# Performance work log

Measured on AMD Instinct MI355X. Metric: run time of the kernel, lower is better.

The kernel has to match this reference:

```python
import jax, jax.numpy as jnp
import numpy as np

B, L, E, H, W = 2, 4096, 512, 8, 128
D = E // H

def _clin(x, Wr, Wi, br, bi):
    # ComplexLinear on real input: out = x@(Wr + i*Wi)^T + (br + i*bi)
    return x @ Wr.T + br, x @ Wi.T + bi

def setup_inputs() -> dict:
    key = jax.random.key(0)
    ks = jax.random.split(key, 20)
    s = 0.02
    d = {
        'query': jax.random.normal(ks[0], (B, L, E), jnp.float32),
        'key':   jax.random.normal(ks[1], (B, L, E), jnp.float32),
        'value': jax.random.normal(ks[2], (B, L, E), jnp.float32),
    }
    names = ['q', 'k', 'v', 'o']
    i = 3
    for n in names:
        d[n + 'Wr'] = jax.random.normal(ks[i], (E, E), jnp.float32) * s; i += 1
        d[n + 'Wi'] = jax.random.normal(ks[i], (E, E), jnp.float32) * s; i += 1
        d[n + 'br'] = jnp.zeros((E,), jnp.float32)
        d[n + 'bi'] = jnp.zeros((E,), jnp.float32)
    return d

def reference(query, key, value,
              qWr, qWi, qbr, qbi,
              kWr, kWi, kbr, kbi,
              vWr, vWi, vbr, vbi,
              oWr, oWi, obr, obi):
    # complex projections (real input -> complex output, kept as (re, im) float pairs)
    qr, qi = _clin(query, qWr, qWi, qbr, qbi)
    kr, ki = _clin(key,   kWr, kWi, kbr, kbi)
    vr, _vi = _clin(value, vWr, vWi, vbr, vbi)  # imag part of V is discarded by the real cast

    def heads(x):
        return x.reshape(B, L, H, D).transpose(0, 2, 1, 3)  # [B,H,L,D]
    qr, qi, kr, ki, vr = map(heads, (qr, qi, kr, ki, vr))

    # Re(q @ k^H) = qr@kr^T + qi@ki^T  (only the real part is ever used)
    scale = 1.0 / np.sqrt(D)
    scores = (jnp.einsum('bhld,bhmd->bhlm', qr, kr)
              + jnp.einsum('bhld,bhmd->bhlm', qi, ki)) * scale

    # Faithful to source: only lower_mask is applied (window_mask is built but never added).
    idx = jnp.arange(L)
    lower_mask = jnp.where(idx[:, None] - idx[None, :] >= W + 1,
                           -jnp.inf, 0.0).astype(scores.dtype)
    probs = jax.nn.softmax(scores + lower_mask, axis=-1)

    # out = probs @ v; cast to query.dtype keeps only Re = probs @ vr
    o = jnp.einsum('bhlm,bhmd->bhld', probs, vr)
    o = o.transpose(0, 2, 1, 3).reshape(B, L, E)

    out_r = o @ oWr.T + obr
    out_i = o @ oWi.T + obi
    return out_r, out_i
```

## Files before the change

kernel.cpp:

```cpp
#include <hip/hip_runtime.h>


typedef unsigned short u16;
typedef unsigned int u32;
typedef __attribute__((ext_vector_type(8))) short bf16x8;
typedef __attribute__((ext_vector_type(4))) float f32x4;
typedef __attribute__((ext_vector_type(16))) float f32x16;
typedef __attribute__((ext_vector_type(4))) u32 u32x4;

#define L_ 4096
#define E_ 512
#define M_ 8192

__device__ __forceinline__ u16 f2bf(float f) {
  union { float f; u32 u; } v; v.f = f;
  return (u16)((v.u + 0x7FFFu + ((v.u >> 16) & 1u)) >> 16);
}

__device__ __forceinline__ void gll16(const void* g, void* l) {
  __builtin_amdgcn_global_load_lds(
      (const __attribute__((address_space(1))) u32*)g,
      (__attribute__((address_space(3))) u32*)l, 16, 0, 0);
}

__global__ void cvt_x_kernel(const float* __restrict__ q, const float* __restrict__ k,
                             const float* __restrict__ v,
                             u16* __restrict__ xq, u16* __restrict__ xk, u16* __restrict__ xv) {
  const int total = 3 * (M_ * E_ / 4);
  int stride = gridDim.x * blockDim.x;
  for (int u = blockIdx.x * blockDim.x + threadIdx.x; u < total; u += stride) {
    int mat = u >> 20, e = u & ((1 << 20) - 1);
    const float4 f = ((const float4*)(mat == 0 ? q : mat == 1 ? k : v))[e];
    ushort4 o = make_ushort4(f2bf(f.x), f2bf(f.y), f2bf(f.z), f2bf(f.w));
    *(ushort4*)((mat == 0 ? xq : mat == 1 ? xk : xv) + (size_t)e * 4) = o;
  }
}

struct CPtrs { const float* w[7]; const float* b[7]; };

__global__ void cvt_wb_kernel(CPtrs p, u16* __restrict__ wcat, float* __restrict__ bcat) {
  const int total = 7 * (E_ * E_ / 4);
  int stride = gridDim.x * blockDim.x;
  int t0 = blockIdx.x * blockDim.x + threadIdx.x;
  for (int u = t0; u < total; u += stride) {
    int wi = u >> 16, e = u & 65535;
    const float4 f = ((const float4*)p.w[wi])[e];
    ushort4 o = make_ushort4(f2bf(f.x), f2bf(f.y), f2bf(f.z), f2bf(f.w));
    *(ushort4*)(wcat + (size_t)wi * 262144 + (size_t)e * 4) = o;
  }
  for (int j = t0; j < 3584; j += stride) bcat[j] = p.b[j >> 9][j & 511];
}

__device__ __forceinline__ void gemm128_main(const u16* __restrict__ A, const u16* __restrict__ Bw,
                                             int m0, int n0w, char* sm, f32x4 acc[4][4]) {
  int tid = threadIdx.x;
  int lane = tid & 63, w = tid >> 6;
  int wm = w >> 1, wn = w & 1;
#pragma unroll
  for (int a = 0; a < 4; a++)
#pragma unroll
    for (int b = 0; b < 4; b++)
#pragma unroll
      for (int j = 0; j < 4; j++) acc[a][b][j] = 0.f;

  auto stage = [&](int buf, int ks) {
    char* dst = sm + buf * 16384;
#pragma unroll
    for (int n = 0; n < 2; n++) {
      int u = n * 256 + tid;
      int row = u >> 2, c = u & 3;
      int so = (c ^ (row & 3)) * 16;
      int ldso = (n * 256 + w * 64) * 16;
      gll16((const char*)(A + (size_t)(m0 + row) * 512 + ks * 32) + so, dst + ldso);
      gll16((const char*)(Bw + (size_t)(n0w + row) * 512 + ks * 32) + so, dst + 8192 + ldso);
    }
  };

  stage(0, 0);
  __syncthreads();
  int cur = 0;
  for (int ks = 0; ks < 16; ks++) {
    if (ks < 15) stage(cur ^ 1, ks + 1);
    const char* as = sm + cur * 16384;
    const char* bs = as + 8192;
    bf16x8 af[4], bfr[4];
#pragma unroll
    for (int i = 0; i < 4; i++) {
      int ra = wm * 64 + i * 16 + (lane & 15);
      af[i] = *(const bf16x8*)(as + ra * 64 + (((lane >> 4) * 16) ^ ((ra & 3) << 4)));
      int rb = wn * 64 + i * 16 + (lane & 15);
      bfr[i] = *(const bf16x8*)(bs + rb * 64 + (((lane >> 4) * 16) ^ ((rb & 3) << 4)));
    }
    __builtin_amdgcn_s_setprio(1);
#pragma unroll
    for (int mt = 0; mt < 4; mt++)
#pragma unroll
      for (int nt = 0; nt < 4; nt++)
        acc[mt][nt] = __builtin_amdgcn_mfma_f32_16x16x32_bf16(af[mt], bfr[nt], acc[mt][nt], 0, 0, 0);
    __builtin_amdgcn_s_setprio(0);
    __syncthreads();
    cur ^= 1;
  }
}

__global__ __launch_bounds__(256) void proj_kernel(
    const u16* __restrict__ xq, const u16* __restrict__ xk, const u16* __restrict__ xv,
    const u16* __restrict__ wcat, const float* __restrict__ bcat,
    u16* __restrict__ qrb, u16* __restrict__ qib,
    u16* __restrict__ krb, u16* __restrict__ kib, u16* __restrict__ vtb) {
  __shared__ alignas(16) char sm[32768];
  int bx = blockIdx.x, by = blockIdx.y;
  const u16* A = bx < 8 ? xq : (bx < 16 ? xk : xv);
  int m0 = by * 128, n0w = bx * 128;
  f32x4 acc[4][4];
  gemm128_main(A, wcat, m0, n0w, sm, acc);

  int lane = threadIdx.x & 63, w = threadIdx.x >> 6;
  int wm = w >> 1, wn = w & 1;
  int lL = lane & 15, lH = lane >> 4;
#pragma unroll
  for (int mt = 0; mt < 4; mt++) {
#pragma unroll
    for (int nt = 0; nt < 4; nt++) {
      int n = n0w + wn * 64 + nt * 16 + lL;
      float bias = bcat[n];
      int e = n & 511;
#pragma unroll
      for (int j = 0; j < 4; j++) {
        int m = m0 + wm * 64 + mt * 16 + lH * 4 + j;
        float val = acc[mt][nt][j] + bias;
        int bb = m >> 12, ll = m & 4095;
        if (bx < 16) {
          if (bx < 8) val *= 0.18033688011112042f;
          u16* dst = (bx < 8) ? ((n & 512) ? qib : qrb) : ((n & 512) ? kib : krb);
          dst[((size_t)((bb * 8 + (e >> 6)) * 4096 + ll) << 6) + (e & 63)] = f2bf(val);
        } else {
          vtb[((size_t)((bb * 8 + (e >> 6)) * 64 + (e & 63)) << 12) + ll] = f2bf(val);
        }
      }
    }
  }
}

__global__ __launch_bounds__(256) void oproj_kernel(
    const u16* __restrict__ obf, const u16* __restrict__ wcat, const float* __restrict__ bcat,
    float* __restrict__ out) {
  __shared__ alignas(16) char sm[32768];
  int bx = blockIdx.x, by = blockIdx.y;
  int m0 = by * 128, n0w = 2560 + bx * 128;
  f32x4 acc[4][4];
  gemm128_main(obf, wcat, m0, n0w, sm, acc);

  int lane = threadIdx.x & 63, w = threadIdx.x >> 6;
  int wm = w >> 1, wn = w & 1;
  int lL = lane & 15, lH = lane >> 4;
#pragma unroll
  for (int mt = 0; mt < 4; mt++) {
#pragma unroll
    for (int nt = 0; nt < 4; nt++) {
      int n = n0w + wn * 64 + nt * 16 + lL;
      float bias = bcat[n];
      int nn = n - 2560;
      float* dst = out + ((nn & 512) ? 4194304 : 0) + (nn & 511);
#pragma unroll
      for (int j = 0; j < 4; j++) {
        int m = m0 + wm * 64 + mt * 16 + lH * 4 + j;
        dst[(size_t)m * 512] = acc[mt][nt][j] + bias;
      }
    }
  }
}

__global__ __launch_bounds__(256, 2) void attn_kernel(
    const u16* __restrict__ qrb, const u16* __restrict__ qib,
    const u16* __restrict__ krb, const u16* __restrict__ kib,
    const u16* __restrict__ vtb, u16* __restrict__ obf) {
  __shared__ alignas(16) char sm[3 * 24576];
  int bid = blockIdx.x;
  int bh = bid & 15;
  int q2 = bid >> 4;
  int qt = (q2 < 16) ? q2 : (47 - q2);
  int bb = bh >> 3, hh = bh & 7;
  int i0 = qt << 7;
  int tid = threadIdx.x;
  int lane = tid & 63, w = tid >> 6;
  int lo = lane & 31, hi = lane >> 5;
  int i0w = i0 + w * 32;
  int irow = i0w + lo;

  bf16x8 fqr[4], fqi[4];
  {
    const u16* qp = qrb + ((size_t)(bh * 4096 + irow) << 6) + hi * 8;
    const u16* qip = qib + ((size_t)(bh * 4096 + irow) << 6) + hi * 8;
#pragma unroll
    for (int c = 0; c < 4; c++) {
      fqr[c] = *(const bf16x8*)(qp + c * 16);
      fqi[c] = *(const bf16x8*)(qip + c * 16);
    }
  }

  f32x16 oa0, oa1;
#pragma unroll
  for (int r = 0; r < 16; r++) { oa0[r] = 0.f; oa1[r] = 0.f; }
  float m_run = -1e30f, l_run = 0.f;

  int jstart = (i0 >= 128) ? (i0 - 128) : 0;
  int ntiles = (4096 - jstart) >> 6;

  auto stage = [&](char* dst, int j0) {
#pragma unroll
    for (int n = 0; n < 2; n++) {
      int u = n * 256 + tid;
      int row = u >> 3, c = u & 7;
      int so = (c ^ (row & 7)) * 16;
      int ldso = (n * 256 + w * 64) * 16;
      size_t krow = ((size_t)(bh * 4096 + j0 + row) << 6);
      gll16((const char*)(krb + krow) + so, dst + ldso);
      gll16((const char*)(kib + krow) + so, dst + 8192 + ldso);
      size_t vrow = ((size_t)(bh * 64 + row) << 12) + j0;
      gll16((const char*)(vtb + vrow) + so, dst + 16384 + ldso);
    }
  };

  int swz = (lo & 7) << 4;

  auto qk = [&](const char* Kbase, f32x16& s0, f32x16& s1) {
    const char* Kr = Kbase;
    const char* Ki = Kbase + 8192;
#pragma unroll
    for (int r = 0; r < 16; r++) { s0[r] = 0.f; s1[r] = 0.f; }
#pragma unroll
    for (int c = 0; c < 4; c++) {
      int off = (c * 32 + hi * 16) ^ swz;
      bf16x8 a0r = *(const bf16x8*)(Kr + lo * 128 + off);
      bf16x8 a0i = *(const bf16x8*)(Ki + lo * 128 + off);
      bf16x8 a1r = *(const bf16x8*)(Kr + (32 + lo) * 128 + off);
      bf16x8 a1i = *(const bf16x8*)(Ki + (32 + lo) * 128 + off);
      __builtin_amdgcn_s_setprio(1);
      s0 = __builtin_amdgcn_mfma_f32_32x32x16_bf16(a0r, fqr[c], s0, 0, 0, 0);
      s1 = __builtin_amdgcn_mfma_f32_32x32x16_bf16(a1r, fqr[c], s1, 0, 0, 0);
      s0 = __builtin_amdgcn_mfma_f32_32x32x16_bf16(a0i, fqi[c], s0, 0, 0, 0);
      s1 = __builtin_amdgcn_mfma_f32_32x32x16_bf16(a1i, fqi[c], s1, 0, 0, 0);
      __builtin_amdgcn_s_setprio(0);
    }
  };

  auto cvtpk = [](float a, float b) -> u32 {
    u32 r;
    asm("v_cvt_pk_bf16_f32 %0, %1, %2" : "=v"(r) : "v"(a), "v"(b));
    return r;
  };
  auto mkfrag = [&](const float* p, bf16x8& fA, bf16x8& fB) {
    u32 x0 = cvtpk(p[0], p[1]), y0 = cvtpk(p[4], p[5]);
    u32 x1 = cvtpk(p[2], p[3]), y1 = cvtpk(p[6], p[7]);
    u32 x2 = cvtpk(p[8], p[9]), y2 = cvtpk(p[12], p[13]);
    u32 x3 = cvtpk(p[10], p[11]), y3 = cvtpk(p[14], p[15]);
    asm("v_permlane32_swap_b32 %0, %1" : "+v"(x0), "+v"(y0));
    asm("v_permlane32_swap_b32 %0, %1" : "+v"(x1), "+v"(y1));
    asm("v_permlane32_swap_b32 %0, %1" : "+v"(x2), "+v"(y2));
    asm("v_permlane32_swap_b32 %0, %1" : "+v"(x3), "+v"(y3));
    u32x4 a; a[0] = x0; a[1] = x1; a[2] = y0; a[3] = y1;
    u32x4 b; b[0] = x2; b[1] = x3; b[2] = y2; b[3] = y3;
    fA = __builtin_bit_cast(bf16x8, a);
    fB = __builtin_bit_cast(bf16x8, b);
  };

  auto smpv = [&](const char* Kbase, int j0, f32x16& s0, f32x16& s1) {
    if (j0 <= i0w - 98) {
#pragma unroll
      for (int r = 0; r < 16; r++) {
        int kk = j0 + (r & 3) + ((r >> 2) << 3) + (hi << 2);
        if (kk <= irow - 129) s0[r] = -3e38f;
        if (kk + 32 <= irow - 129) s1[r] = -3e38f;
      }
    }
    float m4[8];
#pragma unroll
    for (int j = 0; j < 4; j++)
      m4[j] = fmaxf(fmaxf(s0[4 * j], s0[4 * j + 1]), fmaxf(s0[4 * j + 2], s0[4 * j + 3]));
#pragma unroll
    for (int j = 0; j < 4; j++)
      m4[4 + j] = fmaxf(fmaxf(s1[4 * j], s1[4 * j + 1]), fmaxf(s1[4 * j + 2], s1[4 * j + 3]));
    float pmax = fmaxf(fmaxf(fmaxf(m4[0], m4[1]), fmaxf(m4[2], m4[3])),
                       fmaxf(fmaxf(m4[4], m4[5]), fmaxf(m4[6], m4[7])));
    pmax = fmaxf(pmax, __shfl_xor(pmax, 32));

    if (!__all(pmax <= m_run + 11.5f)) {
      float mnew = fmaxf(m_run, pmax);
      float scl = exp2f(m_run - mnew);
#pragma unroll
      for (int r = 0; r < 16; r++) { oa0[r] *= scl; oa1[r] *= scl; }
      l_run *= scl;
      m_run = mnew;
    }

    float ps0 = 0.f, ps1 = 0.f, ps2 = 0.f, ps3 = 0.f;
#pragma unroll
    for (int r = 0; r < 16; r += 4) {
      s0[r] = exp2f(s0[r] - m_run);     ps0 += s0[r];
      s0[r + 1] = exp2f(s0[r + 1] - m_run); ps1 += s0[r + 1];
      s0[r + 2] = exp2f(s0[r + 2] - m_run); ps2 += s0[r + 2];
      s0[r + 3] = exp2f(s0[r + 3] - m_run); ps3 += s0[r + 3];
    }
#pragma unroll
    for (int r = 0; r < 16; r += 4) {
      s1[r] = exp2f(s1[r] - m_run);     ps0 += s1[r];
      s1[r + 1] = exp2f(s1[r + 1] - m_run); ps1 += s1[r + 1];
      s1[r + 2] = exp2f(s1[r + 2] - m_run); ps2 += s1[r + 2];
      s1[r + 3] = exp2f(s1[r + 3] - m_run); ps3 += s1[r + 3];
    }
    float psum = (ps0 + ps1) + (ps2 + ps3);
    psum += __shfl_xor(psum, 32);
    l_run += psum;

    bf16x8 pf0, pf1, pf2, pf3;
    mkfrag((const float*)&s0, pf0, pf1);
    mkfrag((const float*)&s1, pf2, pf3);

    const char* Vt = Kbase + 16384;
#pragma unroll
    for (int kc = 0; kc < 4; kc++) {
      int off = (kc * 32 + hi * 16) ^ swz;
      bf16x8 av0 = *(const bf16x8*)(Vt + lo * 128 + off);
      bf16x8 av1 = *(const bf16x8*)(Vt + (32 + lo) * 128 + off);
      bf16x8 pk = (kc == 0) ? pf0 : (kc == 1) ? pf1 : (kc == 2) ? pf2 : pf3;
      __builtin_amdgcn_s_setprio(1);
      oa0 = __builtin_amdgcn_mfma_f32_32x32x16_bf16(av0, pk, oa0, 0, 0, 0);
      oa1 = __builtin_amdgcn_mfma_f32_32x32x16_bf16(av1, pk, oa1, 0, 0, 0);
      __builtin_amdgcn_s_setprio(0);
    }
  };

  char* cur = sm;
  char* nxt = sm + 24576;
  char* nx2 = sm + 49152;

  stage(cur, jstart);
  stage(nxt, jstart + 64);
  __syncthreads();

  f32x16 sA0, sA1, sB0, sB1;
  qk(cur, sA0, sA1);

  for (int t = 0; t < ntiles; t += 2) {
    int j0 = jstart + (t << 6);
    if (t + 2 < ntiles) stage(nx2, j0 + 128);
    qk(nxt, sB0, sB1);
    smpv(cur, j0, sA0, sA1);
    __syncthreads();
    { char* tmp = cur; cur = nxt; nxt = nx2; nx2 = tmp; }
    if (t + 3 < ntiles) stage(nx2, j0 + 192);
    if (t + 2 < ntiles) qk(nxt, sA0, sA1);
    smpv(cur, j0 + 64, sB0, sB1);
    __syncthreads();
    { char* tmp = cur; cur = nxt; nxt = nx2; nx2 = tmp; }
  }

  float rl = 1.0f / l_run;
  u16* orow = obf + ((size_t)(bb * 4096 + irow) << 9) + hh * 64;
#pragma unroll
  for (int g = 0; g < 4; g++) {
    ushort4 v0 = make_ushort4(f2bf(oa0[4 * g] * rl), f2bf(oa0[4 * g + 1] * rl),
                              f2bf(oa0[4 * g + 2] * rl), f2bf(oa0[4 * g + 3] * rl));
    *(ushort4*)(orow + g * 8 + hi * 4) = v0;
    ushort4 v1 = make_ushort4(f2bf(oa1[4 * g] * rl), f2bf(oa1[4 * g + 1] * rl),
                              f2bf(oa1[4 * g + 2] * rl), f2bf(oa1[4 * g + 3] * rl));
    *(ushort4*)(orow + 32 + g * 8 + hi * 4) = v1;
  }
}

extern "C" void kernel_launch(void* const* d_in, const int* in_sizes, int n_in,
                              void* d_out, int out_size, void* d_ws, size_t ws_size,
                              hipStream_t stream) {
  (void)in_sizes; (void)n_in; (void)out_size; (void)ws_size;
  const float* q = (const float*)d_in[0];
  const float* k = (const float*)d_in[1];
  const float* v = (const float*)d_in[2];
  char* ws = (char*)d_ws;
  u16* wcat = (u16*)(ws + 0x000000);
  float* bcat = (float*)(ws + 0x400000);
  u16* xq  = (u16*)(ws + 0x500000);
  u16* xk  = (u16*)(ws + 0xD00000);
  u16* xv  = (u16*)(ws + 0x1500000);
  u16* qrb = (u16*)(ws + 0x1D00000);
  u16* qib = (u16*)(ws + 0x2500000);
  u16* krb = (u16*)(ws + 0x2D00000);
  u16* kib = (u16*)(ws + 0x3500000);
  u16* vtb = (u16*)(ws + 0x3D00000);
  u16* obf = xq;
  float* out = (float*)d_out;

  cvt_x_kernel<<<2048, 256, 0, stream>>>(q, k, v, xq, xk, xv);

  CPtrs cp;
  cp.w[0] = (const float*)d_in[3];  cp.w[1] = (const float*)d_in[4];
  cp.w[2] = (const float*)d_in[7];  cp.w[3] = (const float*)d_in[8];
  cp.w[4] = (const float*)d_in[11]; cp.w[5] = (const float*)d_in[15]; cp.w[6] = (const float*)d_in[16];
  cp.b[0] = (const float*)d_in[5];  cp.b[1] = (const float*)d_in[6];
  cp.b[2] = (const float*)d_in[9];  cp.b[3] = (const float*)d_in[10];
  cp.b[4] = (const float*)d_in[13]; cp.b[5] = (const float*)d_in[17]; cp.b[6] = (const float*)d_in[18];
  cvt_wb_kernel<<<448, 256, 0, stream>>>(cp, wcat, bcat);

  proj_kernel<<<dim3(20, 64), 256, 0, stream>>>(xq, xk, xv, wcat, bcat, qrb, qib, krb, kib, vtb);
  attn_kernel<<<512, 256, 0, stream>>>(qrb, qib, krb, kib, vtb, obf);
  oproj_kernel<<<dim3(8, 64), 256, 0, stream>>>(obf, wcat, bcat, out);
}
```

Baseline: 197.5 us.

## Run two staggered warp groups per attention block and merge softmax partials

The attention kernel now runs with 512 threads per block, as two groups of four waves. Each group walks the key tiles through a three-slot LDS ring, with the second group lagging one tile behind the first. At the end the two groups merge their partial outputs and running max/sum statistics through shared memory before writing bf16 output. The aim is more waves per CU to hide latency. However, both groups appear to process every tile for the same query rows, which doubles the compute. The launch bound of 512 threads with 4 blocks per CU also tightens the register budget, so spilling is a risk.

```diff
diff --git a/kernel.cpp b/kernel.cpp
--- a/kernel.cpp
+++ b/kernel.cpp
@@ -171,7 +171,7 @@
   }
 }
 
-__global__ __launch_bounds__(256, 2) void attn_kernel(
+__global__ __launch_bounds__(512, 4) void attn_kernel(
     const u16* __restrict__ qrb, const u16* __restrict__ qib,
     const u16* __restrict__ krb, const u16* __restrict__ kib,
     const u16* __restrict__ vtb, u16* __restrict__ obf) {
@@ -184,8 +184,9 @@
   int i0 = qt << 7;
   int tid = threadIdx.x;
   int lane = tid & 63, w = tid >> 6;
+  int grp = w >> 2, wq = w & 3;
   int lo = lane & 31, hi = lane >> 5;
-  int i0w = i0 + w * 32;
+  int i0w = i0 + wq * 32;
   int irow = i0w + lo;
 
   bf16x8 fqr[4], fqi[4];
@@ -205,21 +206,17 @@
   float m_run = -1e30f, l_run = 0.f;
 
   int jstart = (i0 >= 128) ? (i0 - 128) : 0;
-  int ntiles = (4096 - jstart) >> 6;
+  int nt = (4096 - jstart) >> 6;
 
   auto stage = [&](char* dst, int j0) {
-#pragma unroll
-    for (int n = 0; n < 2; n++) {
-      int u = n * 256 + tid;
-      int row = u >> 3, c = u & 7;
-      int so = (c ^ (row & 7)) * 16;
-      int ldso = (n * 256 + w * 64) * 16;
-      size_t krow = ((size_t)(bh * 4096 + j0 + row) << 6);
-      gll16((const char*)(krb + krow) + so, dst + ldso);
-      gll16((const char*)(kib + krow) + so, dst + 8192 + ldso);
-      size_t vrow = ((size_t)(bh * 64 + row) << 12) + j0;
-      gll16((const char*)(vtb + vrow) + so, dst + 16384 + ldso);
-    }
+    int row = tid >> 3, c = tid & 7;
+    int so = (c ^ (row & 7)) * 16;
+    char* ldst = dst + w * 1024;
+    size_t krow = ((size_t)(bh * 4096 + j0 + row) << 6);
+    gll16((const char*)(krb + krow) + so, ldst);
+    gll16((const char*)(kib + krow) + so, ldst + 8192);
+    size_t vrow = ((size_t)(bh * 64 + row) << 12) + j0;
+    gll16((const char*)(vtb + vrow) + so, ldst + 16384);
   };
 
   int swz = (lo & 7) << 4;
@@ -331,41 +328,59 @@
     }
   };
 
-  char* cur = sm;
-  char* nxt = sm + 24576;
-  char* nx2 = sm + 49152;
-
-  stage(cur, jstart);
-  stage(nxt, jstart + 64);
+  stage(sm, jstart);
   __syncthreads();
 
-  f32x16 sA0, sA1, sB0, sB1;
-  qk(cur, sA0, sA1);
-
-  for (int t = 0; t < ntiles; t += 2) {
-    int j0 = jstart + (t << 6);
-    if (t + 2 < ntiles) stage(nx2, j0 + 128);
-    qk(nxt, sB0, sB1);
-    smpv(cur, j0, sA0, sA1);
+  int sslot = 1, cslot = 0;
+  for (int p = 0; p <= nt; p++) {
+    if (p + 1 < nt) {
+      stage(sm + sslot * 24576, jstart + ((p + 1) << 6));
+      sslot = (sslot == 2) ? 0 : sslot + 1;
+    }
+    int myt = p - grp;
+    if (myt >= 0 && myt < nt) {
+      char* base = sm + cslot * 24576;
+      f32x16 s0, s1;
+      qk(base, s0, s1);
+      smpv(base, jstart + (myt << 6), s0, s1);
+      cslot = (cslot == 2) ? 0 : cslot + 1;
+    }
     __syncthreads();
-    { char* tmp = cur; cur = nxt; nxt = nx2; nx2 = tmp; }
-    if (t + 3 < ntiles) stage(nx2, j0 + 192);
-    if (t + 2 < ntiles) qk(nxt, sA0, sA1);
-    smpv(cur, j0 + 64, sB0, sB1);
-    __syncthreads();
-    { char* tmp = cur; cur = nxt; nxt = nx2; nx2 = tmp; }
-  }
-
-  float rl = 1.0f / l_run;
-  u16* orow = obf + ((size_t)(bb * 4096 + irow) << 9) + hh * 64;
-#pragma unroll
-  for (int g = 0; g < 4; g++) {
-    ushort4 v0 = make_ushort4(f2bf(oa0[4 * g] * rl), f2bf(oa0[4 * g + 1] * rl),
-                              f2bf(oa0[4 * g + 2] * rl), f2bf(oa0[4 * g + 3] * rl));
-    *(ushort4*)(orow + g * 8 + hi * 4) = v0;
-    ushort4 v1 = make_ushort4(f2bf(oa1[4 * g] * rl), f2bf(oa1[4 * g + 1] * rl),
-                              f2bf(oa1[4 * g + 2] * rl), f2bf(oa1[4 * g + 3] * rl));
-    *(ushort4*)(orow + 32 + g * 8 + hi * 4) = v1;
+  }
+
+  int msw = (lane & 7) << 4;
+  if (grp == 1) {
+    char* base = sm + wq * 8192;
+#pragma unroll
+    for (int j = 0; j < 8; j++) {
+      f32x4 v;
+#pragma unroll
+      for (int e = 0; e < 4; e++) v[e] = (j < 4) ? oa0[(j & 3) * 4 + e] : oa1[(j & 3) * 4 + e];
+      *(f32x4*)(base + lane * 128 + ((j * 16) ^ msw)) = v;
+    }
+    *(float2*)(sm + 32768 + ((size_t)(wq * 64 + lane) * 8)) = make_float2(m_run, l_run);
+  }
+  __syncthreads();
+  if (grp == 0) {
+    char* base = sm + wq * 8192;
+    float2 ml = *(float2*)(sm + 32768 + ((size_t)(wq * 64 + lane) * 8));
+    float m = fmaxf(m_run, ml.x);
+    float sa = exp2f(m_run - m), sb = exp2f(ml.x - m);
+    float rl = 1.0f / (l_run * sa + ml.y * sb);
+    sa *= rl; sb *= rl;
+    u16* orow = obf + ((size_t)(bb * 4096 + irow) << 9) + hh * 64;
+#pragma unroll
+    for (int j = 0; j < 8; j++) {
+      f32x4 vb = *(const f32x4*)(base + lane * 128 + ((j * 16) ^ msw));
+      float o0 = (j < 4) ? oa0[(j & 3) * 4 + 0] : oa1[(j & 3) * 4 + 0];
+      float o1 = (j < 4) ? oa0[(j & 3) * 4 + 1] : oa1[(j & 3) * 4 + 1];
+      float o2 = (j < 4) ? oa0[(j & 3) * 4 + 2] : oa1[(j & 3) * 4 + 2];
+      float o3 = (j < 4) ? oa0[(j & 3) * 4 + 3] : oa1[(j & 3) * 4 + 3];
+      ushort4 ov = make_ushort4(f2bf(o0 * sa + vb[0] * sb), f2bf(o1 * sa + vb[1] * sb),
+                                f2bf(o2 * sa + vb[2] * sb), f2bf(o3 * sa + vb[3] * sb));
+      int doff = ((j < 4) ? (j * 8) : (32 + (j - 4) * 8)) + hi * 4;
+      *(ushort4*)(orow + doff) = ov;
+    }
   }
 }
 
@@ -402,6 +417,6 @@
   cvt_wb_kernel<<<448, 256, 0, stream>>>(cp, wcat, bcat);
 
   proj_kernel<<<dim3(20, 64), 256, 0, stream>>>(xq, xk, xv, wcat, bcat, qrb, qib, krb, kib, vtb);
-  attn_kernel<<<512, 256, 0, stream>>>(qrb, qib, krb, kib, vtb, obf);
+  attn_kernel<<<512, 512, 0, stream>>>(qrb, qib, krb, kib, vtb, obf);
   oproj_kernel<<<dim3(8, 64), 256, 0, stream>>>(obf, wcat, bcat, out);
 }
```

After: 297.5 us. +50.6%, slower.
